# Kernel optimization log

Measured on AMD Instinct MI355X. Metric: run time of the kernel, lower is better.

The kernel has to match this reference:

```python
import jax, jax.numpy as jnp
import numpy as np

N, E, F_IN, C1, H1, C2, NUM_CLASSES, NUM_GRAPHS = 50000, 800000, 128, 64, 4, 128, 5, 32
NEG_SLOPE = 0.2


def gat_conv(x, W, att_src, att_dst, bias, src, dst, heads, out_ch):
    # x: [N, in], W: [in, heads*out_ch], att_*: [heads, out_ch], bias: [heads*out_ch]
    n = x.shape[0]
    h = (x @ W).reshape(n, heads, out_ch)                      # [N,H,C]
    a_src = jnp.sum(h * att_src, axis=-1)                      # [N,H]
    a_dst = jnp.sum(h * att_dst, axis=-1)                      # [N,H]
    alpha = a_src[src] + a_dst[dst]                            # [E,H]
    alpha = jax.nn.leaky_relu(alpha, NEG_SLOPE)
    # scatter-softmax over incoming edges of each dst node (every node has a self-loop)
    amax = jax.ops.segment_max(alpha, dst, num_segments=n)
    ealpha = jnp.exp(alpha - amax[dst])
    denom = jax.ops.segment_sum(ealpha, dst, num_segments=n)
    alpha = ealpha / (denom[dst] + 1e-16)                      # [E,H]
    msg = h[src] * alpha[..., None]                            # [E,H,C]
    out = jax.ops.segment_sum(msg, dst, num_segments=n)        # [N,H,C]
    return out.reshape(n, heads * out_ch) + bias


def setup_inputs() -> dict:
    key = jax.random.key(0)
    ks = jax.random.split(key, 12)
    x = jax.random.normal(ks[0], (N, F_IN), dtype=jnp.float32)
    edge_index = jax.random.randint(ks[1], (2, E), 0, N, dtype=jnp.int64)
    batch = jnp.sort(jax.random.randint(ks[2], (N,), 0, NUM_GRAPHS, dtype=jnp.int64))
    s1 = 1.0 / np.sqrt(F_IN)
    s2 = 1.0 / np.sqrt(H1 * C1)
    s3 = 1.0 / np.sqrt(C2)
    return {
        "x": x,
        "edge_index": edge_index,
        "batch": batch,
        "W1": jax.random.normal(ks[3], (F_IN, H1 * C1), dtype=jnp.float32) * s1,
        "att_src1": jax.random.normal(ks[4], (H1, C1), dtype=jnp.float32) * s1,
        "att_dst1": jax.random.normal(ks[5], (H1, C1), dtype=jnp.float32) * s1,
        "b1": jnp.zeros((H1 * C1,), dtype=jnp.float32),
        "W2": jax.random.normal(ks[6], (H1 * C1, C2), dtype=jnp.float32) * s2,
        "att_src2": jax.random.normal(ks[7], (1, C2), dtype=jnp.float32) * s2,
        "att_dst2": jax.random.normal(ks[8], (1, C2), dtype=jnp.float32) * s2,
        "b2": jnp.zeros((C2,), dtype=jnp.float32),
        "lin_w": jax.random.normal(ks[9], (C2, NUM_CLASSES), dtype=jnp.float32) * s3,
        "lin_b": jnp.zeros((NUM_CLASSES,), dtype=jnp.float32),
    }


def reference(x, edge_index, batch, W1, att_src1, att_dst1, b1, W2, att_src2, att_dst2, b2, lin_w, lin_b):
    n = x.shape[0]
    # PyG GATConv adds self-loops by default
    loops = jnp.arange(n, dtype=edge_index.dtype)
    src = jnp.concatenate([edge_index[0], loops])
    dst = jnp.concatenate([edge_index[1], loops])
    h = jax.nn.elu(gat_conv(x, W1, att_src1, att_dst1, b1, src, dst, H1, C1))
    h = jax.nn.elu(gat_conv(h, W2, att_src2, att_dst2, b2, src, dst, 1, C2))
    # global_mean_pool over graphs
    sums = jax.ops.segment_sum(h, batch, num_segments=NUM_GRAPHS)          # [G,C2]
    counts = jax.ops.segment_sum(jnp.ones((n,), h.dtype), batch, num_segments=NUM_GRAPHS)
    pooled = sums / jnp.maximum(counts, 1.0)[:, None]
    # dropout is identity in eval mode
    return pooled @ lin_w + lin_b
```

## Files before the change

### kernel.cpp

```cpp
#include <hip/hip_runtime.h>
#include <math.h>

#define NEG_SLOPE 0.2f

__device__ inline float lrelu(float x) { return x > 0.f ? x : NEG_SLOPE * x; }

typedef __attribute__((ext_vector_type(8))) _Float16 f16x8;
typedef __attribute__((ext_vector_type(4))) float f32x4;
typedef __attribute__((ext_vector_type(2))) float f32x2;
typedef __attribute__((ext_vector_type(4))) _Float16 h16x4;
typedef __attribute__((ext_vector_type(2))) _Float16 h16x2;

__global__ void convW_k(const float* __restrict__ W1, const float* __restrict__ W2,
                        _Float16* __restrict__ BT1, _Float16* __restrict__ BT2)
{
    int i = blockIdx.x * blockDim.x + threadIdx.x;
    if (i < 32768) {
        int n = i >> 7, k = i & 127;
        BT1[(size_t)n * 128 + k] = (_Float16)W1[(size_t)k * 256 + n];
    } else {
        int idx = i - 32768;
        int n = idx >> 8, k = idx & 255;
        BT2[(size_t)n * 256 + k] = (_Float16)W2[(size_t)k * 128 + n];
    }
}

template<int N, int K, int H, bool AF16>
__launch_bounds__(256)
__global__ void gemm_fused(const void* __restrict__ A, const _Float16* __restrict__ BT,
                           unsigned char* __restrict__ HB, const float* __restrict__ att_s,
                           const float* __restrict__ att_d, float* __restrict__ aS,
                           float* __restrict__ aD, int M)
{
    constexpr int ITERS = K / 32;
    constexpr int WN = N / 4;
    constexpr int NT = WN / 16;
    constexpr int NCH = (N * 4) / 256;
    __shared__ unsigned short As[64 * 40] __attribute__((aligned(16)));
    __shared__ unsigned short Bs[N * 40] __attribute__((aligned(16)));
    const int t = threadIdx.x;
    const int wave = t >> 6, lane = t & 63;
    const int quad = lane >> 4, l15 = lane & 15;
    const int rowBase = blockIdx.x * 64;

    f32x4 acc[4][NT];
#pragma unroll
    for (int mi = 0; mi < 4; ++mi)
#pragma unroll
        for (int ni = 0; ni < NT; ++ni)
            acc[mi][ni] = (f32x4){0.f, 0.f, 0.f, 0.f};

    const int ar = t >> 2;
    const int ak = (t & 3) << 3;
    const int bc = (t * NCH) >> 2;
    const int bks = (t * NCH) & 3;

    for (int it = 0; it < ITERS; ++it) {
        {
            int gr = rowBase + ar;
            f16x8 hv;
#pragma unroll
            for (int j = 0; j < 8; ++j) hv[j] = (_Float16)0.f;
            if (gr < M) {
                if constexpr (AF16) {
                    hv = *(const f16x8*)((const _Float16*)A + (size_t)gr * K + it * 32 + ak);
                } else {
                    const float* ap = (const float*)A + (size_t)gr * K + it * 32 + ak;
                    float4 v0 = *(const float4*)ap;
                    float4 v1 = *(const float4*)(ap + 4);
                    hv[0] = (_Float16)v0.x; hv[1] = (_Float16)v0.y;
                    hv[2] = (_Float16)v0.z; hv[3] = (_Float16)v0.w;
                    hv[4] = (_Float16)v1.x; hv[5] = (_Float16)v1.y;
                    hv[6] = (_Float16)v1.z; hv[7] = (_Float16)v1.w;
                }
            }
            *(f16x8*)&As[ar * 40 + ak] = hv;
        }
        {
            const _Float16* bp = BT + (size_t)bc * K + it * 32 + bks * 8;
            unsigned short* dp = &Bs[bc * 40 + bks * 8];
#pragma unroll
            for (int j = 0; j < NCH; ++j)
                *(f16x8*)(dp + j * 8) = *(const f16x8*)(bp + j * 8);
        }
        __syncthreads();
        f16x8 af[4], bfr[NT];
#pragma unroll
        for (int mi = 0; mi < 4; ++mi)
            af[mi] = *(const f16x8*)&As[(mi * 16 + l15) * 40 + quad * 8];
#pragma unroll
        for (int ni = 0; ni < NT; ++ni)
            bfr[ni] = *(const f16x8*)&Bs[(wave * WN + ni * 16 + l15) * 40 + quad * 8];
#pragma unroll
        for (int mi = 0; mi < 4; ++mi)
#pragma unroll
            for (int ni = 0; ni < NT; ++ni)
                acc[mi][ni] = __builtin_amdgcn_mfma_f32_16x16x32_f16(
                    af[mi], bfr[ni], acc[mi][ni], 0, 0, 0);
        __syncthreads();
    }
    float asv[NT], adv[NT];
#pragma unroll
    for (int ni = 0; ni < NT; ++ni) {
        int col = wave * WN + ni * 16 + l15;
        asv[ni] = att_s[col];
        adv[ni] = att_d[col];
    }
#pragma unroll
    for (int mi = 0; mi < 4; ++mi) {
#pragma unroll
        for (int r = 0; r < 4; ++r) {
            int row = rowBase + mi * 16 + quad * 4 + r;
            bool ok = row < M;
            float ss = 0.f, sd = 0.f;
#pragma unroll
            for (int ni = 0; ni < NT; ++ni) {
                float v = acc[mi][ni][r];
                ss += v * asv[ni];
                sd += v * adv[ni];
            }
#pragma unroll
            for (int ni = 0; ni < NT; ni += 2) {
                int pk = __builtin_amdgcn_cvt_pk_fp8_f32(acc[mi][ni][r],
                                                         acc[mi][ni + 1][r], 0, false);
                if (ok) {
                    HB[(size_t)row * N + wave * WN + ni * 16 + l15] =
                        (unsigned char)(pk & 0xff);
                    HB[(size_t)row * N + wave * WN + (ni + 1) * 16 + l15] =
                        (unsigned char)((pk >> 8) & 0xff);
                }
            }
#pragma unroll
            for (int off = 8; off > 0; off >>= 1) {
                ss += __shfl_xor(ss, off);
                sd += __shfl_xor(sd, off);
            }
            if (ok && l15 == 0) {
                if (H == 4) {
                    aS[row * 4 + wave] = ss;
                    aD[row * 4 + wave] = sd;
                } else {
                    atomicAdd(&aS[row], ss);
                    atomicAdd(&aD[row], sd);
                }
            }
        }
    }
}

__global__ void count_k(const int* __restrict__ dst, int* __restrict__ counts, int E, int Nn)
{
    int e = blockIdx.x * blockDim.x + threadIdx.x;
    if (e >= E + Nn) return;
    int d = (e < E) ? dst[e] : (e - E);
    atomicAdd(&counts[d], 1);
}

__global__ void scan1_k(const int* __restrict__ counts, int* __restrict__ partial,
                        int* __restrict__ bsum, int Nn)
{
    __shared__ int sh[256];
    int i = blockIdx.x * 256 + threadIdx.x;
    int v = (i < Nn) ? counts[i] : 0;
    sh[threadIdx.x] = v;
    __syncthreads();
#pragma unroll
    for (int o = 1; o < 256; o <<= 1) {
        int t = (threadIdx.x >= o) ? sh[threadIdx.x - o] : 0;
        __syncthreads();
        sh[threadIdx.x] += t;
        __syncthreads();
    }
    if (i < Nn) partial[i] = sh[threadIdx.x] - v;
    if (threadIdx.x == 255) bsum[blockIdx.x] = sh[255];
}

__global__ void scan2_k(int* __restrict__ bsum, int nb)
{
    __shared__ int sh[256];
    int v = (threadIdx.x < nb) ? bsum[threadIdx.x] : 0;
    sh[threadIdx.x] = v;
    __syncthreads();
#pragma unroll
    for (int o = 1; o < 256; o <<= 1) {
        int t = (threadIdx.x >= o) ? sh[threadIdx.x - o] : 0;
        __syncthreads();
        sh[threadIdx.x] += t;
        __syncthreads();
    }
    if (threadIdx.x < nb) bsum[threadIdx.x] = sh[threadIdx.x] - v;
}

__global__ void scan3_k(const int* __restrict__ partial, const int* __restrict__ bsum,
                        int* __restrict__ rowptr, int* __restrict__ ccursor, int Nn, int ET)
{
    int i = blockIdx.x * 256 + threadIdx.x;
    if (i < Nn) {
        int v = partial[i] + bsum[i >> 8];
        rowptr[i] = v;
        if ((i & 63) == 0) ccursor[i >> 6] = v;
    }
    if (i == Nn) rowptr[Nn] = ET;
}

#define BIN_EPT 32
__launch_bounds__(256)
__global__ void binpass_k(const int* __restrict__ src, const int* __restrict__ dst,
                          int* __restrict__ ccursor, unsigned int* __restrict__ tmp,
                          int ET, int E, int NBUCK)
{
    __shared__ int hist[1024];
    for (int i = threadIdx.x; i < NBUCK; i += 256) hist[i] = 0;
    __syncthreads();
    int e0 = blockIdx.x * (256 * BIN_EPT) + threadIdx.x;
    unsigned int ev[BIN_EPT];
    int meta[BIN_EPT];
#pragma unroll
    for (int j = 0; j < BIN_EPT; ++j) {
        int e = e0 + j * 256;
        meta[j] = -1;
        if (e < ET) {
            int s, d;
            if (e < E) { s = src[e]; d = dst[e]; } else { s = e - E; d = s; }
            ev[j] = (unsigned int)s | ((unsigned int)d << 16);
            int b = d >> 6;
            int r = atomicAdd(&hist[b], 1);
            meta[j] = (r << 10) | b;
        }
    }
    __syncthreads();
    for (int i = threadIdx.x; i < NBUCK; i += 256) {
        int c = hist[i];
        hist[i] = (c > 0) ? atomicAdd(&ccursor[i], c) : 0;
    }
    __syncthreads();
#pragma unroll
    for (int j = 0; j < BIN_EPT; ++j) {
        if (meta[j] >= 0) {
            int b = meta[j] & 1023;
            int r = meta[j] >> 10;
            tmp[hist[b] + r] = ev[j];
        }
    }
}

__global__ void fine_k(const int* __restrict__ rowptr, const unsigned int* __restrict__ tmp,
                       unsigned short* __restrict__ esrc, int Nn)
{
    __shared__ int lcur[64];
    int n0 = blockIdx.x << 6;
    int nend = min(n0 + 64, Nn);
    if (threadIdx.x < 64) {
        int n = n0 + threadIdx.x;
        lcur[threadIdx.x] = (n < Nn) ? rowptr[n] : 0;
    }
    __syncthreads();
    int base = rowptr[n0];
    int end = rowptr[nend];
    for (int i = base + (int)threadIdx.x; i < end; i += 256) {
        unsigned int v = tmp[i];
        int nl = (v >> 16) & 63;
        int pos = atomicAdd(&lcur[nl], 1);
        esrc[pos] = (unsigned short)(v & 0xffffu);
    }
}

__global__ void gather1_k(const int* __restrict__ rp, const unsigned short* __restrict__ esrc,
                          const unsigned char* __restrict__ hb, const float* __restrict__ aS,
                          const float* __restrict__ aD, const float* __restrict__ bias,
                          _Float16* __restrict__ out, int Nn)
{
    int d = blockIdx.x * 4 + (threadIdx.x >> 6);
    int lane = threadIdx.x & 63;
    if (d >= Nn) return;
    int c4 = lane << 2;
    int head = lane >> 4;
    int p0 = __builtin_amdgcn_readfirstlane(rp[d]);
    int p1 = __builtin_amdgcn_readfirstlane(rp[d + 1]);
    float adh = aD[d * 4 + head];
    const float* aSh = aS + head;
    float m = -1e30f, den = 0.f;
    float ax = 0.f, ay = 0.f, az = 0.f, aw = 0.f;
    int p = p0;
    for (; p + 8 <= p1; p += 8) {
        int s[8];
        float l[8];
#pragma unroll
        for (int j = 0; j < 8; ++j) s[j] = __builtin_amdgcn_readfirstlane(esrc[p + j]);
#pragma unroll
        for (int j = 0; j < 8; ++j) l[j] = lrelu(aSh[s[j] * 4] + adh);
        float lm = l[0];
#pragma unroll
        for (int j = 1; j < 8; ++j) lm = fmaxf(lm, l[j]);
        if (lm > m) {
            float r = __expf(m - lm);
            ax *= r; ay *= r; az *= r; aw *= r; den *= r;
            m = lm;
        }
        unsigned int v[8];
#pragma unroll
        for (int j = 0; j < 8; ++j)
            v[j] = *(const unsigned int*)&hb[(size_t)s[j] * 256 + c4];
#pragma unroll
        for (int j = 0; j < 8; ++j) {
            float w = __expf(l[j] - m);
            den += w;
            f32x2 lo = __builtin_amdgcn_cvt_pk_f32_fp8((int)v[j], false);
            f32x2 hi = __builtin_amdgcn_cvt_pk_f32_fp8((int)v[j], true);
            ax += lo[0] * w;
            ay += lo[1] * w;
            az += hi[0] * w;
            aw += hi[1] * w;
        }
    }
    for (; p < p1; ++p) {
        int s0 = __builtin_amdgcn_readfirstlane(esrc[p]);
        float l0 = lrelu(aSh[s0 * 4] + adh);
        if (l0 > m) {
            float r = __expf(m - l0);
            ax *= r; ay *= r; az *= r; aw *= r; den *= r;
            m = l0;
        }
        float w0 = __expf(l0 - m);
        den += w0;
        unsigned int v0 = *(const unsigned int*)&hb[(size_t)s0 * 256 + c4];
        f32x2 lo = __builtin_amdgcn_cvt_pk_f32_fp8((int)v0, false);
        f32x2 hi = __builtin_amdgcn_cvt_pk_f32_fp8((int)v0, true);
        ax += lo[0] * w0; ay += lo[1] * w0;
        az += hi[0] * w0; aw += hi[1] * w0;
    }
    float inv = 1.f / (den + 1e-16f);
    float4 b4 = *(const float4*)&bias[c4];
    float rx, ry, rz, rw;
    rx = ax * inv + b4.x; rx = rx > 0.f ? rx : expm1f(rx);
    ry = ay * inv + b4.y; ry = ry > 0.f ? ry : expm1f(ry);
    rz = az * inv + b4.z; rz = rz > 0.f ? rz : expm1f(rz);
    rw = aw * inv + b4.w; rw = rw > 0.f ? rw : expm1f(rw);
    h16x4 r16;
    r16[0] = (_Float16)rx; r16[1] = (_Float16)ry;
    r16[2] = (_Float16)rz; r16[3] = (_Float16)rw;
    *(h16x4*)&out[(size_t)d * 256 + c4] = r16;
}

__global__ void gather2_k(const int* __restrict__ rp, const unsigned short* __restrict__ esrc,
                          const unsigned char* __restrict__ hb, const float* __restrict__ aS,
                          const float* __restrict__ aD, _Float16* __restrict__ out, int Nn)
{
    int d = blockIdx.x * 4 + (threadIdx.x >> 6);
    int lane = threadIdx.x & 63;
    if (d >= Nn) return;
    int c2 = lane << 1;
    int p0 = __builtin_amdgcn_readfirstlane(rp[d]);
    int p1 = __builtin_amdgcn_readfirstlane(rp[d + 1]);
    float adh = aD[d];
    float m = -1e30f, den = 0.f;
    float ax = 0.f, ay = 0.f;
    int p = p0;
    for (; p + 8 <= p1; p += 8) {
        int s[8];
        float l[8];
#pragma unroll
        for (int j = 0; j < 8; ++j) s[j] = __builtin_amdgcn_readfirstlane(esrc[p + j]);
#pragma unroll
        for (int j = 0; j < 8; ++j) l[j] = lrelu(aS[s[j]] + adh);
        float lm = l[0];
#pragma unroll
        for (int j = 1; j < 8; ++j) lm = fmaxf(lm, l[j]);
        if (lm > m) {
            float r = __expf(m - lm);
            ax *= r; ay *= r; den *= r;
            m = lm;
        }
        unsigned short v[8];
#pragma unroll
        for (int j = 0; j < 8; ++j)
            v[j] = *(const unsigned short*)&hb[(size_t)s[j] * 128 + c2];
#pragma unroll
        for (int j = 0; j < 8; ++j) {
            float w = __expf(l[j] - m);
            den += w;
            f32x2 lo = __builtin_amdgcn_cvt_pk_f32_fp8((int)v[j], false);
            ax += lo[0] * w;
            ay += lo[1] * w;
        }
    }
    for (; p < p1; ++p) {
        int s0 = __builtin_amdgcn_readfirstlane(esrc[p]);
        float l0 = lrelu(aS[s0] + adh);
        if (l0 > m) {
            float r = __expf(m - l0);
            ax *= r; ay *= r; den *= r;
            m = l0;
        }
        float w0 = __expf(l0 - m);
        den += w0;
        unsigned short v0 = *(const unsigned short*)&hb[(size_t)s0 * 128 + c2];
        f32x2 lo = __builtin_amdgcn_cvt_pk_f32_fp8((int)v0, false);
        ax += lo[0] * w0;
        ay += lo[1] * w0;
    }
    float inv = 1.f / (den + 1e-16f);
    h16x2 r16;
    r16[0] = (_Float16)(ax * inv);
    r16[1] = (_Float16)(ay * inv);
    *(h16x2*)&out[(size_t)d * 128 + c2] = r16;
}

__global__ void pool_k(const _Float16* __restrict__ o2, const float* __restrict__ b2,
                       const int* __restrict__ batch, float* __restrict__ sums, int Nn, int C)
{
    int c = threadIdx.x;
    int n0 = blockIdx.x * 64;
    int n1 = min(n0 + 64, Nn);
    float local = 0.f;
    int gcur = batch[n0];
    float bc = b2[c];
    for (int n = n0; n < n1; ++n) {
        int g = batch[n];
        if (g != gcur) {
            atomicAdd(&sums[gcur * C + c], local);
            local = 0.f;
            gcur = g;
        }
        float v = (float)o2[(size_t)n * C + c] + bc;
        local += v > 0.f ? v : expm1f(v);
    }
    atomicAdd(&sums[gcur * C + c], local);
}

__global__ void final_k(const float* __restrict__ sums, const int* __restrict__ batch,
                        const float* __restrict__ lin_w, const float* __restrict__ lin_b,
                        float* __restrict__ out, int Nn, int G, int C, int NC)
{
    __shared__ float inv[64];
    int t = threadIdx.x;
    if (t < G) {
        int lo = 0, hi = Nn;
        while (lo < hi) { int mid = (lo + hi) >> 1; if (batch[mid] < t) lo = mid + 1; else hi = mid; }
        int lb = lo;
        lo = 0; hi = Nn;
        while (lo < hi) { int mid = (lo + hi) >> 1; if (batch[mid] < t + 1) lo = mid + 1; else hi = mid; }
        int cnt = lo - lb;
        inv[t] = 1.f / fmaxf((float)cnt, 1.f);
    }
    __syncthreads();
    if (t < G * NC) {
        int g = t / NC, k = t % NC;
        float acc = 0.f;
        for (int c = 0; c < C; ++c) acc += sums[g * C + c] * lin_w[c * NC + k];
        out[t] = acc * inv[g] + lin_b[k];
    }
}

extern "C" void kernel_launch(void* const* d_in, const int* in_sizes, int n_in,
                              void* d_out, int out_size, void* d_ws, size_t ws_size,
                              hipStream_t stream)
{
    const float* x      = (const float*)d_in[0];
    const int*   eidx   = (const int*)d_in[1];
    const int*   batch  = (const int*)d_in[2];
    const float* W1     = (const float*)d_in[3];
    const float* att_s1 = (const float*)d_in[4];
    const float* att_d1 = (const float*)d_in[5];
    const float* b1     = (const float*)d_in[6];
    const float* W2     = (const float*)d_in[7];
    const float* att_s2 = (const float*)d_in[8];
    const float* att_d2 = (const float*)d_in[9];
    const float* b2     = (const float*)d_in[10];
    const float* lin_w  = (const float*)d_in[11];
    const float* lin_b  = (const float*)d_in[12];

    const int Nn  = in_sizes[2];
    const int E   = in_sizes[1] / 2;
    const int H1_ = 4, C1_ = 64, C2_ = 128, G = 32, NC = 5;
    const int D1 = H1_ * C1_;
    const int ET = E + Nn;
    const int NBUCK = (Nn + 63) >> 6;

    const int* srcp = eidx;
    const int* dstp = eidx + E;

    float* ws = (float*)d_ws;
    size_t off = 0;
    auto alloc = [&](size_t n) { float* p = ws + off; off += n; return p; };
    _Float16* o1h = (_Float16*)alloc((size_t)Nn * D1 / 2);
    _Float16* o2h = (_Float16*)alloc((size_t)Nn * C2_ / 2);
    float* aS1  = alloc((size_t)Nn * H1_);
    float* aD1  = alloc((size_t)Nn * H1_);
    float* aS2  = alloc(Nn);
    float* aD2  = alloc(Nn);
    float* sums = alloc((size_t)G * C2_);
    _Float16* BT1 = (_Float16*)alloc(D1 * 128 / 2);
    _Float16* BT2 = (_Float16*)alloc(C2_ * 256 / 2);
    unsigned char* hb1 = (unsigned char*)alloc((size_t)Nn * D1 / 4);
    unsigned char* hb2 = (unsigned char*)alloc((size_t)Nn * C2_ / 4);
    int* iws    = (int*)(ws + off);
    int* counts = iws;
    int* partial= iws + Nn;
    int* rowptr = iws + 2 * Nn;
    int* bsum   = iws + 3 * Nn + 1;
    int* ccursor= iws + 3 * Nn + 1 + 256;
    unsigned int* tmp = (unsigned int*)(iws + 3 * Nn + 1 + 256 + 1024);
    unsigned short* esrc = (unsigned short*)(tmp + ET);

    const int NB = (Nn + 255) / 256;
    const int GB = (Nn + 63) / 64;
    const int BINB = (ET + 256 * BIN_EPT - 1) / (256 * BIN_EPT);

    hipMemsetAsync(counts, 0, (size_t)Nn * 4, stream);
    hipMemsetAsync(aS2, 0, (size_t)2 * Nn * 4, stream);
    count_k<<<(ET + 255) / 256, 256, 0, stream>>>(dstp, counts, E, Nn);
    scan1_k<<<NB, 256, 0, stream>>>(counts, partial, bsum, Nn);
    scan2_k<<<1, 256, 0, stream>>>(bsum, NB);
    scan3_k<<<(Nn + 256) / 256, 256, 0, stream>>>(partial, bsum, rowptr, ccursor, Nn, ET);
    binpass_k<<<BINB, 256, 0, stream>>>(srcp, dstp, ccursor, tmp, ET, E, NBUCK);
    fine_k<<<NBUCK, 256, 0, stream>>>(rowptr, tmp, esrc, Nn);

    convW_k<<<256, 256, 0, stream>>>(W1, W2, BT1, BT2);

    gemm_fused<256, 128, 4, false><<<GB, 256, 0, stream>>>(x, BT1, hb1, att_s1, att_d1,
                                                           aS1, aD1, Nn);
    gather1_k<<<(Nn + 3) / 4, 256, 0, stream>>>(rowptr, esrc, hb1, aS1, aD1, b1, o1h, Nn);

    gemm_fused<128, 256, 1, true><<<GB, 256, 0, stream>>>(o1h, BT2, hb2, att_s2, att_d2,
                                                          aS2, aD2, Nn);
    gather2_k<<<(Nn + 3) / 4, 256, 0, stream>>>(rowptr, esrc, hb2, aS2, aD2, o2h, Nn);

    hipMemsetAsync(sums, 0, (size_t)G * C2_ * 4, stream);
    pool_k<<<GB, C2_, 0, stream>>>(o2h, b2, batch, sums, Nn, C2_);
    final_k<<<1, 256, 0, stream>>>(sums, batch, lin_w, lin_b, (float*)d_out, Nn, G, C2_, NC);
}
```

Measured before the change: 347.9 us.

## Build CSR from bucket-level counts and derive per-node rowptr inside fine pass

Replaces per-node global atomic counting and the three-kernel scan with a shared-memory bucket histogram (64 nodes per bucket), a single-block bucket scan, and a per-bucket local count and scan inside fine_k that writes rowptr. This cuts global atomics and the number of kernel launches in CSR construction. Separately, the gather kernels drop their scalar tail loops and handle the remainder with a clamped, masked 8-wide batch. That trades a few redundant loads for a more uniform loop.

```diff
diff --git a/kernel.cpp b/kernel.cpp
--- a/kernel.cpp
+++ b/kernel.cpp
@@ -148,62 +148,53 @@
     }
 }
 
-__global__ void count_k(const int* __restrict__ dst, int* __restrict__ counts, int E, int Nn)
-{
-    int e = blockIdx.x * blockDim.x + threadIdx.x;
-    if (e >= E + Nn) return;
-    int d = (e < E) ? dst[e] : (e - E);
-    atomicAdd(&counts[d], 1);
-}
-
-__global__ void scan1_k(const int* __restrict__ counts, int* __restrict__ partial,
-                        int* __restrict__ bsum, int Nn)
-{
-    __shared__ int sh[256];
-    int i = blockIdx.x * 256 + threadIdx.x;
-    int v = (i < Nn) ? counts[i] : 0;
-    sh[threadIdx.x] = v;
-    __syncthreads();
-#pragma unroll
-    for (int o = 1; o < 256; o <<= 1) {
-        int t = (threadIdx.x >= o) ? sh[threadIdx.x - o] : 0;
+#define BIN_EPT 32
+__launch_bounds__(256)
+__global__ void bcount_k(const int* __restrict__ dst, int* __restrict__ bcnt,
+                         int ET, int E, int NBUCK)
+{
+    __shared__ int hist[1024];
+    for (int i = threadIdx.x; i < NBUCK; i += 256) hist[i] = 0;
+    __syncthreads();
+    int e0 = blockIdx.x * (256 * BIN_EPT) + threadIdx.x;
+#pragma unroll
+    for (int j = 0; j < BIN_EPT; ++j) {
+        int e = e0 + j * 256;
+        if (e < ET) {
+            int d = (e < E) ? dst[e] : (e - E);
+            atomicAdd(&hist[d >> 6], 1);
+        }
+    }
+    __syncthreads();
+    for (int i = threadIdx.x; i < NBUCK; i += 256) {
+        int c = hist[i];
+        if (c > 0) atomicAdd(&bcnt[i], c);
+    }
+}
+
+__global__ void bscan_k(const int* __restrict__ bcnt, int* __restrict__ bbase,
+                        int* __restrict__ ccursor, int nb)
+{
+    __shared__ int sh[1024];
+    int t = threadIdx.x;
+    int v = (t < nb) ? bcnt[t] : 0;
+    sh[t] = v;
+    __syncthreads();
+#pragma unroll
+    for (int o = 1; o < 1024; o <<= 1) {
+        int u = (t >= o) ? sh[t - o] : 0;
         __syncthreads();
-        sh[threadIdx.x] += t;
+        sh[t] += u;
         __syncthreads();
     }
-    if (i < Nn) partial[i] = sh[threadIdx.x] - v;
-    if (threadIdx.x == 255) bsum[blockIdx.x] = sh[255];
-}
-
-__global__ void scan2_k(int* __restrict__ bsum, int nb)
-{
-    __shared__ int sh[256];
-    int v = (threadIdx.x < nb) ? bsum[threadIdx.x] : 0;
-    sh[threadIdx.x] = v;
-    __syncthreads();
-#pragma unroll
-    for (int o = 1; o < 256; o <<= 1) {
-        int t = (threadIdx.x >= o) ? sh[threadIdx.x - o] : 0;
-        __syncthreads();
-        sh[threadIdx.x] += t;
-        __syncthreads();
-    }
-    if (threadIdx.x < nb) bsum[threadIdx.x] = sh[threadIdx.x] - v;
-}
-
-__global__ void scan3_k(const int* __restrict__ partial, const int* __restrict__ bsum,
-                        int* __restrict__ rowptr, int* __restrict__ ccursor, int Nn, int ET)
-{
-    int i = blockIdx.x * 256 + threadIdx.x;
-    if (i < Nn) {
-        int v = partial[i] + bsum[i >> 8];
-        rowptr[i] = v;
-        if ((i & 63) == 0) ccursor[i >> 6] = v;
-    }
-    if (i == Nn) rowptr[Nn] = ET;
-}
-
-#define BIN_EPT 32
+    if (t < nb) {
+        int excl = sh[t] - v;
+        bbase[t] = excl;
+        ccursor[t] = excl;
+    }
+    if (t == nb - 1) bbase[nb] = sh[t];
+}
+
 __launch_bounds__(256)
 __global__ void binpass_k(const int* __restrict__ src, const int* __restrict__ dst,
                           int* __restrict__ ccursor, unsigned int* __restrict__ tmp,
@@ -244,23 +235,43 @@
     }
 }
 
-__global__ void fine_k(const int* __restrict__ rowptr, const unsigned int* __restrict__ tmp,
-                       unsigned short* __restrict__ esrc, int Nn)
-{
-    __shared__ int lcur[64];
-    int n0 = blockIdx.x << 6;
-    int nend = min(n0 + 64, Nn);
-    if (threadIdx.x < 64) {
-        int n = n0 + threadIdx.x;
-        lcur[threadIdx.x] = (n < Nn) ? rowptr[n] : 0;
-    }
-    __syncthreads();
-    int base = rowptr[n0];
-    int end = rowptr[nend];
-    for (int i = base + (int)threadIdx.x; i < end; i += 256) {
+__global__ void fine_k(const int* __restrict__ bbase, const unsigned int* __restrict__ tmp,
+                       int* __restrict__ rowptr, unsigned short* __restrict__ esrc,
+                       int Nn, int ET, int NBUCK)
+{
+    __shared__ int lcnt[64], lpre[64], lcur[64];
+    int t = threadIdx.x;
+    int b = blockIdx.x;
+    int n0 = b << 6;
+    int base = bbase[b];
+    int end = bbase[b + 1];
+    if (t < 64) lcnt[t] = 0;
+    __syncthreads();
+    for (int i = base + t; i < end; i += 256)
+        atomicAdd(&lcnt[(tmp[i] >> 16) & 63], 1);
+    __syncthreads();
+    if (t < 64) lpre[t] = lcnt[t];
+    __syncthreads();
+#pragma unroll
+    for (int o = 1; o < 64; o <<= 1) {
+        int u = (t < 64 && t >= o) ? lpre[t - o] : 0;
+        __syncthreads();
+        if (t < 64) lpre[t] += u;
+        __syncthreads();
+    }
+    if (t < 64) {
+        int n = n0 + t;
+        int excl = lpre[t] - lcnt[t];
+        if (n < Nn) {
+            rowptr[n] = base + excl;
+            lcur[t] = base + excl;
+        }
+    }
+    if (b == NBUCK - 1 && t == 0) rowptr[Nn] = ET;
+    __syncthreads();
+    for (int i = base + t; i < end; i += 256) {
         unsigned int v = tmp[i];
-        int nl = (v >> 16) & 63;
-        int pos = atomicAdd(&lcur[nl], 1);
+        int pos = atomicAdd(&lcur[(v >> 16) & 63], 1);
         esrc[pos] = (unsigned short)(v & 0xffffu);
     }
 }
@@ -281,14 +292,21 @@
     const float* aSh = aS + head;
     float m = -1e30f, den = 0.f;
     float ax = 0.f, ay = 0.f, az = 0.f, aw = 0.f;
-    int p = p0;
-    for (; p + 8 <= p1; p += 8) {
+    for (int p = p0; p < p1; p += 8) {
+        int nv = p1 - p;
         int s[8];
         float l[8];
 #pragma unroll
-        for (int j = 0; j < 8; ++j) s[j] = __builtin_amdgcn_readfirstlane(esrc[p + j]);
-#pragma unroll
-        for (int j = 0; j < 8; ++j) l[j] = lrelu(aSh[s[j] * 4] + adh);
+        for (int j = 0; j < 8; ++j) {
+            int e = p + j;
+            e = e < p1 ? e : p1 - 1;
+            s[j] = __builtin_amdgcn_readfirstlane(esrc[e]);
+        }
+#pragma unroll
+        for (int j = 0; j < 8; ++j) {
+            float lj = lrelu(aSh[s[j] * 4] + adh);
+            l[j] = (j < nv) ? lj : -1e30f;
+        }
         float lm = l[0];
 #pragma unroll
         for (int j = 1; j < 8; ++j) lm = fmaxf(lm, l[j]);
@@ -312,22 +330,6 @@
             az += hi[0] * w;
             aw += hi[1] * w;
         }
-    }
-    for (; p < p1; ++p) {
-        int s0 = __builtin_amdgcn_readfirstlane(esrc[p]);
-        float l0 = lrelu(aSh[s0 * 4] + adh);
-        if (l0 > m) {
-            float r = __expf(m - l0);
-            ax *= r; ay *= r; az *= r; aw *= r; den *= r;
-            m = l0;
-        }
-        float w0 = __expf(l0 - m);
-        den += w0;
-        unsigned int v0 = *(const unsigned int*)&hb[(size_t)s0 * 256 + c4];
-        f32x2 lo = __builtin_amdgcn_cvt_pk_f32_fp8((int)v0, false);
-        f32x2 hi = __builtin_amdgcn_cvt_pk_f32_fp8((int)v0, true);
-        ax += lo[0] * w0; ay += lo[1] * w0;
-        az += hi[0] * w0; aw += hi[1] * w0;
     }
     float inv = 1.f / (den + 1e-16f);
     float4 b4 = *(const float4*)&bias[c4];
@@ -355,14 +357,21 @@
     float adh = aD[d];
     float m = -1e30f, den = 0.f;
     float ax = 0.f, ay = 0.f;
-    int p = p0;
-    for (; p + 8 <= p1; p += 8) {
+    for (int p = p0; p < p1; p += 8) {
+        int nv = p1 - p;
         int s[8];
         float l[8];
 #pragma unroll
-        for (int j = 0; j < 8; ++j) s[j] = __builtin_amdgcn_readfirstlane(esrc[p + j]);
-#pragma unroll
-        for (int j = 0; j < 8; ++j) l[j] = lrelu(aS[s[j]] + adh);
+        for (int j = 0; j < 8; ++j) {
+            int e = p + j;
+            e = e < p1 ? e : p1 - 1;
+            s[j] = __builtin_amdgcn_readfirstlane(esrc[e]);
+        }
+#pragma unroll
+        for (int j = 0; j < 8; ++j) {
+            float lj = lrelu(aS[s[j]] + adh);
+            l[j] = (j < nv) ? lj : -1e30f;
+        }
         float lm = l[0];
 #pragma unroll
         for (int j = 1; j < 8; ++j) lm = fmaxf(lm, l[j]);
@@ -383,21 +392,6 @@
             ax += lo[0] * w;
             ay += lo[1] * w;
         }
-    }
-    for (; p < p1; ++p) {
-        int s0 = __builtin_amdgcn_readfirstlane(esrc[p]);
-        float l0 = lrelu(aS[s0] + adh);
-        if (l0 > m) {
-            float r = __expf(m - l0);
-            ax *= r; ay *= r; den *= r;
-            m = l0;
-        }
-        float w0 = __expf(l0 - m);
-        den += w0;
-        unsigned short v0 = *(const unsigned short*)&hb[(size_t)s0 * 128 + c2];
-        f32x2 lo = __builtin_amdgcn_cvt_pk_f32_fp8((int)v0, false);
-        ax += lo[0] * w0;
-        ay += lo[1] * w0;
     }
     float inv = 1.f / (den + 1e-16f);
     h16x2 r16;
@@ -495,26 +489,22 @@
     unsigned char* hb1 = (unsigned char*)alloc((size_t)Nn * D1 / 4);
     unsigned char* hb2 = (unsigned char*)alloc((size_t)Nn * C2_ / 4);
     int* iws    = (int*)(ws + off);
-    int* counts = iws;
-    int* partial= iws + Nn;
-    int* rowptr = iws + 2 * Nn;
-    int* bsum   = iws + 3 * Nn + 1;
-    int* ccursor= iws + 3 * Nn + 1 + 256;
-    unsigned int* tmp = (unsigned int*)(iws + 3 * Nn + 1 + 256 + 1024);
+    int* rowptr = iws;
+    int* bcnt   = iws + Nn + 1;
+    int* bbase  = iws + Nn + 1 + 1024;
+    int* ccursor= iws + Nn + 1 + 2049;
+    unsigned int* tmp = (unsigned int*)(iws + Nn + 1 + 2049 + 1024);
     unsigned short* esrc = (unsigned short*)(tmp + ET);
 
-    const int NB = (Nn + 255) / 256;
     const int GB = (Nn + 63) / 64;
     const int BINB = (ET + 256 * BIN_EPT - 1) / (256 * BIN_EPT);
 
-    hipMemsetAsync(counts, 0, (size_t)Nn * 4, stream);
+    hipMemsetAsync(bcnt, 0, 1024 * 4, stream);
     hipMemsetAsync(aS2, 0, (size_t)2 * Nn * 4, stream);
-    count_k<<<(ET + 255) / 256, 256, 0, stream>>>(dstp, counts, E, Nn);
-    scan1_k<<<NB, 256, 0, stream>>>(counts, partial, bsum, Nn);
-    scan2_k<<<1, 256, 0, stream>>>(bsum, NB);
-    scan3_k<<<(Nn + 256) / 256, 256, 0, stream>>>(partial, bsum, rowptr, ccursor, Nn, ET);
+    bcount_k<<<BINB, 256, 0, stream>>>(dstp, bcnt, ET, E, NBUCK);
+    bscan_k<<<1, 1024, 0, stream>>>(bcnt, bbase, ccursor, NBUCK);
     binpass_k<<<BINB, 256, 0, stream>>>(srcp, dstp, ccursor, tmp, ET, E, NBUCK);
-    fine_k<<<NBUCK, 256, 0, stream>>>(rowptr, tmp, esrc, Nn);
+    fine_k<<<NBUCK, 256, 0, stream>>>(bbase, tmp, rowptr, esrc, Nn, ET, NBUCK);
 
     convW_k<<<256, 256, 0, stream>>>(W1, W2, BT1, BT2);
 
```

Result: faster. 338.2 us (-2.8%).
